# Performance work log

Hardware: AMD Instinct MI355X
Metric: run time of the kernel (lower is better)

The kernel has to match this reference:

```python
import jax, jax.numpy as jnp
import numpy as np

T = 32768          # number of t_eval points, dt = 30 s
BATCH = 32         # batched initial conditions
N_ROOMS = 16
N_STATE = N_ROOMS + 2
HID = 16
T0 = 259200.0      # start time (seconds); kept small so fp32 resolves 30 s steps
DT_GRID = 30.0
MU, STD = 23.359, 1.41      # state normalization for policy input
Q_VALUE = -16914.0          # cooling power per unit action
DAY = 86400.0
WEEK = 604800.0
A_SCALE, A_DIAG, B_SCALE = 1e-4, 1e-3, 1e-6


def setup_inputs() -> dict:
    key = jax.random.key(0)
    ks = jax.random.split(key, 8)
    t_eval = (T0 + DT_GRID * jnp.arange(T)).astype(jnp.float32)
    iv = 26.0 + jax.random.normal(ks[0], (BATCH, N_STATE), jnp.float32)
    W_A = jax.random.normal(ks[1], (N_STATE, N_STATE), jnp.float32)
    W_B = jax.random.normal(ks[2], (N_STATE, 1 + N_ROOMS), jnp.float32)
    W1 = jax.random.normal(ks[3], (HID, N_STATE + 2), jnp.float32)
    b1 = jax.random.normal(ks[4], (HID,), jnp.float32)
    w2 = jax.random.normal(ks[5], (HID,), jnp.float32)
    b2 = jax.random.normal(ks[6], (1,), jnp.float32)
    # outside-temperature table on a 30 s grid covering t_eval plus the +600 s tail
    Tout_table = 10.0 + 10.0 * jax.random.uniform(ks[7], (T + 21,), jnp.float32)
    return dict(t_eval=t_eval, iv=iv, W_A=W_A, W_B=W_B, W1=W1, b1=b1,
                w2=w2, b2=b2, Tout_table=Tout_table)


def reference(t_eval, iv, W_A, W_B, W1, b1, w2, b2, Tout_table):
    n = iv.shape[-1]
    A = A_SCALE * W_A - A_DIAG * jnp.eye(n, dtype=W_A.dtype)   # stable dynamics
    Bm = B_SCALE * W_B                                         # [n, 1+n_rooms]
    b_tout = Bm[:, 0]                                          # Tout column of B
    b_rooms = Q_VALUE * jnp.sum(Bm[:, 1:], axis=1)             # B @ (Q*ones) per unit action
    t0 = t_eval[0]
    nT = Tout_table.shape[0]

    def tout(t):  # linear interp of outside temperature at absolute time t
        pos = (t - t0) / DT_GRID
        i = jnp.clip(jnp.floor(pos).astype(jnp.int32), 0, nT - 2)
        fr = pos - i.astype(pos.dtype)
        return (1.0 - fr) * Tout_table[i] + fr * Tout_table[i + 1]

    def policy(t, x):  # deterministic cooling action in (0,1), per batch element
        tod = jnp.mod(t, DAY) / DAY
        tow = jnp.mod(t + 3.0 * DAY, WEEK) / WEEK   # epoch day 0 is a Thursday
        feats = jnp.broadcast_to(jnp.stack([tow, tod]).astype(x.dtype), (x.shape[0], 2))
        s = jnp.concatenate([(x - MU) / STD, feats], axis=1)   # [B, n+2]
        h = jnp.tanh(s @ W1.T + b1)
        return jax.nn.sigmoid(h @ w2 + b2[0])                  # [B]

    def f(t, x, act):  # dx/dt = A x + B u,  u = [Tout, Q*ones(n_rooms)]
        Bu = tout(t) * b_tout[None, :] + act[:, None] * b_rooms[None, :]
        return x @ A.T + Bu

    def step(x, ts):  # one fixed-step RK4 step; action held over the step (>=30 s gate)
        t, tn = ts
        dt = tn - t
        act = policy(t, x)
        k1 = f(t, x, act)
        k2 = f(t + 0.5 * dt, x + 0.5 * dt * k1, act)
        k3 = f(t + 0.5 * dt, x + 0.5 * dt * k2, act)
        k4 = f(tn, x + dt * k3, act)
        xn = x + (dt / 6.0) * (k1 + 2.0 * k2 + 2.0 * k3 + k4)
        return xn, xn

    _, xs = jax.lax.scan(step, iv, (t_eval[:-1], t_eval[1:]))
    return jnp.concatenate([iv[None], xs], axis=0)   # [T, batch, n_state]
```

## Files before the change

kernel.cpp:

```cpp
#include <hip/hip_runtime.h>

#define NSTATE 18
#define NBATCH 32
#define TSTEPS 32768
#define SEGS   64
#define SEGLEN 512
#define BURN   192

typedef float v2f __attribute__((ext_vector_type(2)));

#define PKFMA_LO(ACC, Gp, Xp) \
  asm("v_pk_fma_f32 %0, %1, %2, %0 op_sel:[0,0,0] op_sel_hi:[1,0,1]" \
      : "+v"(ACC) : "v"(Gp), "v"(Xp))
#define PKFMA_HI(ACC, Gp, Xp) \
  asm("v_pk_fma_f32 %0, %1, %2, %0 op_sel:[0,1,0] op_sel_hi:[1,1,1]" \
      : "+v"(ACC) : "v"(Gp), "v"(Xp))

template <int CTRL>
__device__ __forceinline__ float dpp_xadd(float x) {
  int y = __builtin_amdgcn_update_dpp(0, __float_as_int(x), CTRL, 0xF, 0xF, true);
  return x + __int_as_float(y);
}

#define STEPP(XI, XO, TIN, TNX, P, DOSTORE)                                       \
  do {                                                                            \
    TNX = *(const v2f*)(ldsT + 2 * (P) + 2);          \
    float fw = (float)uw, ft = (float)ut;                                         \
    float ilo = fmaf(TIN.x, C0.x, fmaf(TIN.y, C1.x, CBlo));                       \
    ilo = fmaf(fw, CWlo, ilo);                                                    \
    ilo = fmaf(ft, CTlo, ilo);                                                    \
    ilo = fmaf(a0p, F0.x, ilo);                                                   \
    ilo = fmaf(a1p, F1.x, ilo);                                                   \
    float ihi = fmaf(TIN.x, C0.y, TIN.y * C1.y);                                  \
    ihi = fmaf(a0p, F0.y, ihi);                                                   \
    ihi = fmaf(a1p, F1.y, ihi);                                                   \
    ilo = fmaf(TNX.x, C2lo, ilo);         \
    v2f accA; accA.x = ilo; accA.y = ihi;                                         \
    v2f accB; accB.x = 0.0f; accB.y = 0.0f;                                       \
    PKFMA_LO(accA, G[0],  XI[0]);  PKFMA_HI(accB, G[1],  XI[0]);                  \
    PKFMA_LO(accA, G[2],  XI[1]);  PKFMA_HI(accB, G[3],  XI[1]);                  \
    PKFMA_LO(accA, G[4],  XI[2]);  PKFMA_HI(accB, G[5],  XI[2]);                  \
    PKFMA_LO(accA, G[6],  XI[3]);  PKFMA_HI(accB, G[7],  XI[3]);                  \
    PKFMA_LO(accA, G[8],  XI[4]);  PKFMA_HI(accB, G[9],  XI[4]);                  \
    PKFMA_LO(accA, G[10], XI[5]);  PKFMA_HI(accB, G[11], XI[5]);                  \
    PKFMA_LO(accA, G[12], XI[6]);  PKFMA_HI(accB, G[13], XI[6]);                  \
    PKFMA_LO(accA, G[14], XI[7]);  PKFMA_HI(accB, G[15], XI[7]);                  \
    PKFMA_LO(accA, G[16], XI[8]);  PKFMA_HI(accB, G[17], XI[8]);                  \
    v2f acc = accA + accB;                                                        \
    float vlo = acc.x, vhi = acc.y;                                               \
    xbuf[wIdx] = vlo;              \
    XO[0] = *(const v2f*)(xbuf + 0);  XO[1] = *(const v2f*)(xbuf + 2);            \
    XO[2] = *(const v2f*)(xbuf + 4);  XO[3] = *(const v2f*)(xbuf + 6);            \
    XO[4] = *(const v2f*)(xbuf + 8);  XO[5] = *(const v2f*)(xbuf + 10);           \
    XO[6] = *(const v2f*)(xbuf + 12); XO[7] = *(const v2f*)(xbuf + 14);           \
    XO[8] = *(const v2f*)(xbuf + 16);                                             \
    float e2 = exp2f(vlo);                                                        \
    float rc = __builtin_amdgcn_rcpf(1.0f + e2);                                  \
    float pA = fmaf(nw2A, rc, w2A);                                               \
    pA = dpp_xadd<0xB1>(pA); pA = dpp_xadd<0x4E>(pA);                             \
    pA = dpp_xadd<0x141>(pA); pA = dpp_xadd<0x140>(pA);                           \
    float ez = exp2f(fmaf(pA, -1.44269504f, nb2));                                \
    float an = __builtin_amdgcn_rcpf(1.0f + ez);                                  \
    float aj0 = __int_as_float(__builtin_amdgcn_readlane(__float_as_int(an), 32));\
    float qB = fmaf(aj0, uB, vlo);                                                \
    float e2b = exp2f(qB);                                                        \
    float rcb = __builtin_amdgcn_rcpf(1.0f + e2b);                                \
    float pB = fmaf(nw2B, rcb, w2B);                                              \
    pB = dpp_xadd<0xB1>(pB); pB = dpp_xadd<0x4E>(pB);                             \
    pB = dpp_xadd<0x141>(pB); pB = dpp_xadd<0x140>(pB);                           \
    float ezb = exp2f(fmaf(pB, -1.44269504f, nb2));                               \
    float anb = __builtin_amdgcn_rcpf(1.0f + ezb);                                \
    float aj1 = __int_as_float(__builtin_amdgcn_readlane(__float_as_int(anb), 48));\
    if (DOSTORE) {                                                                \
      if (L < NSTATE) {                                                           \
        ob[L] = fmaf(aj0, cact, vhi);                               \
        ob[L + 576] = fmaf(aj1, cact, fmaf(aj0, pcact, vlo));       \
      }                                                                            \
      ob += 1152;                                                                 \
    }                                                                             \
    a0p = aj0; a1p = aj1;                                                         \
    ut += 60u; if (ut >= 86400u) ut -= 86400u;                                    \
    uw += 60u; if (uw >= 604800u) uw -= 604800u;                                  \
  } while (0)

__global__ __launch_bounds__(64) void rc_run(
    const float* __restrict__ WA, const float* __restrict__ WB,
    const float* __restrict__ W1, const float* __restrict__ b1,
    const float* __restrict__ w2, const float* __restrict__ b2,
    const float* __restrict__ iv, const float* __restrict__ tout,
    float* __restrict__ out) {
  __shared__ double DB[1440];
  double* A   = DB;
  double* A2  = DB + 324;
  double* A3  = DB + 648;
  double* A4  = DB + 972;
  double* bt  = DB + 1296;
  double* br  = DB + 1314;
  double* cv  = DB + 1332;
  double* d0v = DB + 1350;
  double* d1v = DB + 1368;
  double* pc1 = DB + 1386;
  double* pc2 = DB + 1404;
  double* pc3 = DB + 1422;
  __shared__ __align__(16) float xbuf[96];

  const int L = threadIdx.x;
  const int idx = blockIdx.x;
  const int b = idx & (NBATCH - 1);
  const int s = idx >> 5;
  const double dt = 30.0;
  const float PS = 2.88539008f;

  const int ks = (s == SEGS - 1) ? (TSTEPS - 1 - SEGLEN) : s * SEGLEN;
  const int kb = max(0, ks - BURN);
  const int mBurn = ks - kb;
  const int mEnd = (ks + SEGLEN) - kb;

  for (int t = L; t < 324; t += 64) {
    int i = t / 18, j = t % 18;
    A[t] = 1e-4 * (double)WA[t] - (i == j ? 1e-3 : 0.0);
  }
  if (L < NSTATE) {
    bt[L] = 1e-6 * (double)WB[L * 17 + 0];
    double ssum = 0.0;
    for (int c = 1; c < 17; ++c) ssum += (double)WB[L * 17 + c];
    br[L] = -16914.0 * 1e-6 * ssum;
  }
  __syncthreads();
  for (int t = L; t < 324; t += 64) {
    int i = t / 18, j = t % 18;
    double s2 = 0.0;
    for (int l = 0; l < 18; ++l) s2 += A[i * 18 + l] * A[l * 18 + j];
    A2[t] = s2;
  }
  __syncthreads();
  for (int t = L; t < 324; t += 64) {
    int i = t / 18, j = t % 18;
    double s3 = 0.0, s4 = 0.0;
    for (int l = 0; l < 18; ++l) {
      s3 += A2[i * 18 + l] * A[l * 18 + j];
      s4 += A2[i * 18 + l] * A2[l * 18 + j];
    }
    A3[t] = s3;
    A4[t] = s4;
  }
  __syncthreads();
  if (L < NSTATE) {
    double sc = 0.0, dd0 = 0.0, dd1 = 0.0;
    for (int j = 0; j < 18; ++j) {
      double m = (dt / 6.0) * ((L == j ? 6.0 : 0.0) + 3.0 * dt * A[L * 18 + j] +
                               dt * dt * A2[L * 18 + j] +
                               0.25 * dt * dt * dt * A3[L * 18 + j]);
      sc += m * br[j];
      double m1 = (dt / 6.0) * ((L == j ? 1.0 : 0.0) + dt * A[L * 18 + j] +
                                0.5 * dt * dt * A2[L * 18 + j] +
                                0.25 * dt * dt * dt * A3[L * 18 + j]);
      double m23 = (dt / 6.0) * ((L == j ? 4.0 : 0.0) + 2.0 * dt * A[L * 18 + j] +
                                 0.5 * dt * dt * A2[L * 18 + j]);
      double m4 = (L == j ? dt / 6.0 : 0.0);
      dd0 += (m1 + 0.5 * m23) * bt[j];
      dd1 += (0.5 * m23 + m4) * bt[j];
    }
    cv[L] = sc;
    d0v[L] = dd0;
    d1v[L] = dd1;
  }
  __syncthreads();
  for (int t = L; t < 324; t += 64) {
    int i = t / 18, j = t % 18;
    A[t] = (i == j ? 1.0 : 0.0) + dt * A[t] + (dt * dt / 2.0) * A2[t] +
           (dt * dt * dt / 6.0) * A3[t] + (dt * dt * dt * dt / 24.0) * A4[t];
  }
  __syncthreads();
  for (int t = L; t < 324; t += 64) {
    int i = t / 18, j = t % 18;
    double s2 = 0.0;
    for (int l = 0; l < 18; ++l) s2 += A[i * 18 + l] * A[l * 18 + j];
    A2[t] = s2;
  }
  __syncthreads();
  if (L < NSTATE) { double s1 = 0.0; for (int j = 0; j < 18; ++j) s1 += A[L * 18 + j] * cv[j];  pc1[L] = s1; }
  __syncthreads();
  if (L < NSTATE) { double s1 = 0.0; for (int j = 0; j < 18; ++j) s1 += A[L * 18 + j] * pc1[j]; pc2[L] = s1; }
  __syncthreads();
  if (L < NSTATE) { double s1 = 0.0; for (int j = 0; j < 18; ++j) s1 += A[L * 18 + j] * pc2[j]; pc3[L] = s1; }
  __syncthreads();

  v2f G[18];
  v2f F0; F0.x = 0.f; F0.y = 0.f;
  v2f F1; F1.x = 0.f; F1.y = 0.f;
  v2f C0; C0.x = 0.f; C0.y = 0.f;
  v2f C1; C1.x = 0.f; C1.y = 0.f;
  float C2lo = 0.f, CWlo = 0.f, CTlo = 0.f, CBlo = 0.f;
  float cact = 0.f, pcact = 0.f, uB = 0.f;
  float w2A = 0.f, nw2A = 0.f, w2B = 0.f, nw2B = 0.f;
  const float b2v = b2[0];
  const float nb2 = -1.44269504f * b2v;

  if (L < NSTATE) {
    for (int j = 0; j < 18; ++j) { G[j].x = (float)A2[L * 18 + j]; G[j].y = (float)A[L * 18 + j]; }
    double pd0 = 0.0, pd1 = 0.0;
    for (int j = 0; j < 18; ++j) { pd0 += A[L * 18 + j] * d0v[j]; pd1 += A[L * 18 + j] * d1v[j]; }
    C0.x = (float)pd0;            C0.y = (float)d0v[L];
    C1.x = (float)(pd1 + d0v[L]); C1.y = (float)d1v[L];
    C2lo = (float)d1v[L];
    F0.x = (float)pc3[L]; F0.y = (float)pc2[L];
    F1.x = (float)pc2[L]; F1.y = (float)pc1[L];
    cact = (float)cv[L];
    pcact = (float)pc1[L];
  } else if (L >= 32 && L < 48) {
    int m = L - 32;
    double f0 = 0.0, f1 = 0.0, ssum = 0.0;
    for (int j = 0; j < 18; ++j) {
      double g = (double)W1[m * 20 + j] * ((double)PS / 1.41);
      G[j].x = (float)g; G[j].y = 0.f;
      f0 += g * pc1[j];
      f1 += g * cv[j];
      ssum += (double)W1[m * 20 + j];
    }
    F0.x = (float)f0; F1.x = (float)f1;
    CBlo = (float)(((double)b1[m] - ssum * (23.359 / 1.41)) * (double)PS);
    CWlo = W1[m * 20 + 18] * PS * (1.0f / 604800.0f);
    CTlo = W1[m * 20 + 19] * PS * (1.0f / 86400.0f);
    w2A = w2[m]; nw2A = -2.0f * w2A;
  } else if (L >= 48) {
    int m = L - 48;
    double f0 = 0.0, f1 = 0.0, ub = 0.0, ssum = 0.0, wd0 = 0.0, wd1 = 0.0;
    for (int j = 0; j < 18; ++j) {
      double g = (double)W1[m * 20 + j] * ((double)PS / 1.41);
      double wp = 0.0;
      for (int k = 0; k < 18; ++k)
        wp += (double)W1[m * 20 + k] * ((double)PS / 1.41) * A[k * 18 + j];
      G[j].x = (float)wp; G[j].y = 0.f;
      f0 += g * pc2[j];
      f1 += g * pc1[j];
      ub += g * cv[j];
      wd0 += g * d0v[j];
      wd1 += g * d1v[j];
      ssum += (double)W1[m * 20 + j];
    }
    F0.x = (float)f0; F1.x = (float)f1; uB = (float)ub;
    C0.x = (float)wd0; C1.x = (float)wd1;
    CWlo = W1[m * 20 + 18] * PS * (1.0f / 604800.0f);
    CTlo = W1[m * 20 + 19] * PS * (1.0f / 86400.0f);
    CBlo = (float)(((double)b1[m] - ssum * (23.359 / 1.41)) * (double)PS) +
           30.0f * CWlo + 30.0f * CTlo;
    w2B = w2[m]; nw2B = -2.0f * w2B;
  } else {
    for (int j = 0; j < 18; ++j) { G[j].x = 0.f; G[j].y = 0.f; }
  }
  __syncthreads();

  float* ldsT = (float*)DB;
  const int cnt = mEnd + 2;
  for (int i = L; i < cnt; i += 64) ldsT[i] = tout[kb + i];
  __syncthreads();

  float q = (L < NSTATE) ? iv[b * NSTATE + L] : 0.0f;
  if (s == 0 && L < NSTATE) out[b * NSTATE + L] = q;

  float a0p = 0.0f, a1p = 0.0f;
  unsigned ut = (30u * (unsigned)kb) % 86400u;
  unsigned uw = (518400u + 30u * (unsigned)kb) % 604800u;

  float* ob = out + (size_t)(ks + 1) * (NBATCH * NSTATE) + b * NSTATE;

  const int wIdx = (L < NSTATE) ? L : (32 + L);
  xbuf[wIdx] = q;
  v2f X[9], Y[9];
  X[0] = *(const v2f*)(xbuf + 0);  X[1] = *(const v2f*)(xbuf + 2);
  X[2] = *(const v2f*)(xbuf + 4);  X[3] = *(const v2f*)(xbuf + 6);
  X[4] = *(const v2f*)(xbuf + 8);  X[5] = *(const v2f*)(xbuf + 10);
  X[6] = *(const v2f*)(xbuf + 12); X[7] = *(const v2f*)(xbuf + 14);
  X[8] = *(const v2f*)(xbuf + 16);

  v2f tU, tV;
  tU.x = ldsT[0]; tU.y = ldsT[1];

  const int nburn = mBurn >> 1;
  const int ntot = mEnd >> 1;
  int p = 0;
  for (; p < nburn; p += 2) {
    STEPP(X, Y, tU, tV, p, false);
    STEPP(Y, X, tV, tU, p + 1, false);
  }
  for (; p < ntot; p += 2) {
    STEPP(X, Y, tU, tV, p, true);
    STEPP(Y, X, tV, tU, p + 1, true);
  }
}

extern "C" void kernel_launch(void* const* d_in, const int* in_sizes, int n_in,
                              void* d_out, int out_size, void* d_ws, size_t ws_size,
                              hipStream_t stream) {
  const float* iv = (const float*)d_in[1];
  const float* WA = (const float*)d_in[2];
  const float* WB = (const float*)d_in[3];
  const float* W1 = (const float*)d_in[4];
  const float* b1 = (const float*)d_in[5];
  const float* w2 = (const float*)d_in[6];
  const float* b2 = (const float*)d_in[7];
  const float* tout = (const float*)d_in[8];
  float* out = (float*)d_out;

  rc_run<<<NBATCH * SEGS, 64, 0, stream>>>(WA, WB, W1, b1, w2, b2, iv, tout, out);
}
```

Measured before the change: 261.6 us.

## Delay action feedback by one extra double-step to shorten the serial critical path

Reworks the recurrence so the state update uses actions from two double-steps back, folded in through precomputed powers of the propagator (pc4, pc5). The most recent actions enter only as a scalar correction to the policy pre-activation and to the stored outputs. This takes the previous step's sigmoid/DPP-reduction chain off the dependency path of the matrix-vector FMA chain, so consecutive steps can overlap. In exchange it adds a few FMAs per step, more setup matrix-vector products, and extra registers.

```diff
diff --git a/kernel.cpp b/kernel.cpp
--- a/kernel.cpp
+++ b/kernel.cpp
@@ -22,19 +22,33 @@
   return x + __int_as_float(y);
 }
 
-#define STEPP(XI, XO, TIN, TNX, P, DOSTORE)                                       \
+#define TAIL(Q, AOUT, W2V, NW2V, LANE)                                            \
+  {                                                                               \
+    float e_ = exp2f(Q);                                                          \
+    float rc_ = __builtin_amdgcn_rcpf(1.0f + e_);                                 \
+    float p_ = fmaf(NW2V, rc_, W2V);                                              \
+    p_ = dpp_xadd<0xB1>(p_);                                                      \
+    p_ = dpp_xadd<0x4E>(p_);                                                      \
+    p_ = dpp_xadd<0x141>(p_);                                                     \
+    p_ = dpp_xadd<0x140>(p_);                                                     \
+    float ez_ = exp2f(fmaf(p_, -1.44269504f, nb2));                               \
+    float an_ = __builtin_amdgcn_rcpf(1.0f + ez_);                                \
+    AOUT = __int_as_float(__builtin_amdgcn_readlane(__float_as_int(an_), LANE));  \
+  }
+
+#define STEPP(XI, XO, TIN, TNX, P, DOSTORE, PP0, PP1, PR0, PR1)                   \
   do {                                                                            \
     TNX = *(const v2f*)(ldsT + 2 * (P) + 2);          \
     float fw = (float)uw, ft = (float)ut;                                         \
     float ilo = fmaf(TIN.x, C0.x, fmaf(TIN.y, C1.x, CBlo));                       \
     ilo = fmaf(fw, CWlo, ilo);                                                    \
     ilo = fmaf(ft, CTlo, ilo);                                                    \
-    ilo = fmaf(a0p, F0.x, ilo);                                                   \
-    ilo = fmaf(a1p, F1.x, ilo);                                                   \
+    ilo = fmaf(PP0, F0.x, ilo);        \
+    ilo = fmaf(PP1, F1.x, ilo);                                                   \
     float ihi = fmaf(TIN.x, C0.y, TIN.y * C1.y);                                  \
-    ihi = fmaf(a0p, F0.y, ihi);                                                   \
-    ihi = fmaf(a1p, F1.y, ihi);                                                   \
-    ilo = fmaf(TNX.x, C2lo, ilo);         \
+    ihi = fmaf(PP0, F0.y, ihi);                                                   \
+    ihi = fmaf(PP1, F1.y, ihi);                                                   \
+    ilo = fmaf(TNX.x, C2lo, ilo);                                                 \
     v2f accA; accA.x = ilo; accA.y = ihi;                                         \
     v2f accB; accB.x = 0.0f; accB.y = 0.0f;                                       \
     PKFMA_LO(accA, G[0],  XI[0]);  PKFMA_HI(accB, G[1],  XI[0]);                  \
@@ -54,31 +68,21 @@
     XO[4] = *(const v2f*)(xbuf + 8);  XO[5] = *(const v2f*)(xbuf + 10);           \
     XO[6] = *(const v2f*)(xbuf + 12); XO[7] = *(const v2f*)(xbuf + 14);           \
     XO[8] = *(const v2f*)(xbuf + 16);                                             \
-    float e2 = exp2f(vlo);                                                        \
-    float rc = __builtin_amdgcn_rcpf(1.0f + e2);                                  \
-    float pA = fmaf(nw2A, rc, w2A);                                               \
-    pA = dpp_xadd<0xB1>(pA); pA = dpp_xadd<0x4E>(pA);                             \
-    pA = dpp_xadd<0x141>(pA); pA = dpp_xadd<0x140>(pA);                           \
-    float ez = exp2f(fmaf(pA, -1.44269504f, nb2));                                \
-    float an = __builtin_amdgcn_rcpf(1.0f + ez);                                  \
-    float aj0 = __int_as_float(__builtin_amdgcn_readlane(__float_as_int(an), 32));\
-    float qB = fmaf(aj0, uB, vlo);                                                \
-    float e2b = exp2f(qB);                                                        \
-    float rcb = __builtin_amdgcn_rcpf(1.0f + e2b);                                \
-    float pB = fmaf(nw2B, rcb, w2B);                                              \
-    pB = dpp_xadd<0xB1>(pB); pB = dpp_xadd<0x4E>(pB);                             \
-    pB = dpp_xadd<0x141>(pB); pB = dpp_xadd<0x140>(pB);                           \
-    float ezb = exp2f(fmaf(pB, -1.44269504f, nb2));                               \
-    float anb = __builtin_amdgcn_rcpf(1.0f + ezb);                                \
-    float aj1 = __int_as_float(__builtin_amdgcn_readlane(__float_as_int(anb), 48));\
+                     \
+    float q0 = fmaf(PR0, PAv.x, fmaf(PR1, PAv.y, vlo));                           \
+    float aj0, aj1;                                                               \
+    TAIL(q0, aj0, w2A, nw2A, 32);                                                 \
+    float qB = fmaf(aj0, uB, q0);                                                 \
+    TAIL(qB, aj1, w2B, nw2B, 48);                                                 \
     if (DOSTORE) {                                                                \
       if (L < NSTATE) {                                                           \
-        ob[L] = fmaf(aj0, cact, vhi);                               \
-        ob[L + 576] = fmaf(aj1, cact, fmaf(aj0, pcact, vlo));       \
-      }                                                                            \
+        ob[L] = fmaf(aj0, cact, fmaf(PR0, Q0.x, fmaf(PR1, Q1.x, vhi)));           \
+        ob[L + 576] = fmaf(aj1, cact,                                             \
+                           fmaf(aj0, pcact, fmaf(PR0, Q0.y, fmaf(PR1, Q1.y, vlo)))); \
+      }                                                                           \
       ob += 1152;                                                                 \
     }                                                                             \
-    a0p = aj0; a1p = aj1;                                                         \
+    PP0 = aj0; PP1 = aj1;         \
     ut += 60u; if (ut >= 86400u) ut -= 86400u;                                    \
     uw += 60u; if (uw >= 604800u) uw -= 604800u;                                  \
   } while (0)
@@ -89,7 +93,7 @@
     const float* __restrict__ w2, const float* __restrict__ b2,
     const float* __restrict__ iv, const float* __restrict__ tout,
     float* __restrict__ out) {
-  __shared__ double DB[1440];
+  __shared__ double DB[1476];
   double* A   = DB;
   double* A2  = DB + 324;
   double* A3  = DB + 648;
@@ -102,6 +106,8 @@
   double* pc1 = DB + 1386;
   double* pc2 = DB + 1404;
   double* pc3 = DB + 1422;
+  double* pc4 = DB + 1440;
+  double* pc5 = DB + 1458;
   __shared__ __align__(16) float xbuf[96];
 
   const int L = threadIdx.x;
@@ -185,10 +191,17 @@
   __syncthreads();
   if (L < NSTATE) { double s1 = 0.0; for (int j = 0; j < 18; ++j) s1 += A[L * 18 + j] * pc2[j]; pc3[L] = s1; }
   __syncthreads();
+  if (L < NSTATE) { double s1 = 0.0; for (int j = 0; j < 18; ++j) s1 += A[L * 18 + j] * pc3[j]; pc4[L] = s1; }
+  __syncthreads();
+  if (L < NSTATE) { double s1 = 0.0; for (int j = 0; j < 18; ++j) s1 += A[L * 18 + j] * pc4[j]; pc5[L] = s1; }
+  __syncthreads();
 
   v2f G[18];
   v2f F0; F0.x = 0.f; F0.y = 0.f;
   v2f F1; F1.x = 0.f; F1.y = 0.f;
+  v2f PAv; PAv.x = 0.f; PAv.y = 0.f;
+  v2f Q0; Q0.x = 0.f; Q0.y = 0.f;
+  v2f Q1; Q1.x = 0.f; Q1.y = 0.f;
   v2f C0; C0.x = 0.f; C0.y = 0.f;
   v2f C1; C1.x = 0.f; C1.y = 0.f;
   float C2lo = 0.f, CWlo = 0.f, CTlo = 0.f, CBlo = 0.f;
@@ -204,42 +217,52 @@
     C0.x = (float)pd0;            C0.y = (float)d0v[L];
     C1.x = (float)(pd1 + d0v[L]); C1.y = (float)d1v[L];
     C2lo = (float)d1v[L];
-    F0.x = (float)pc3[L]; F0.y = (float)pc2[L];
-    F1.x = (float)pc2[L]; F1.y = (float)pc1[L];
+    F0.x = (float)pc5[L]; F0.y = (float)pc4[L];
+    F1.x = (float)pc4[L]; F1.y = (float)pc3[L];
+    Q0.x = (float)pc2[L]; Q0.y = (float)pc3[L];
+    Q1.x = (float)pc1[L]; Q1.y = (float)pc2[L];
     cact = (float)cv[L];
     pcact = (float)pc1[L];
   } else if (L >= 32 && L < 48) {
     int m = L - 32;
-    double f0 = 0.0, f1 = 0.0, ssum = 0.0;
+    double f0 = 0.0, f1 = 0.0, pa0 = 0.0, pa1 = 0.0, ssum = 0.0;
     for (int j = 0; j < 18; ++j) {
       double g = (double)W1[m * 20 + j] * ((double)PS / 1.41);
       G[j].x = (float)g; G[j].y = 0.f;
-      f0 += g * pc1[j];
-      f1 += g * cv[j];
+      f0 += g * pc3[j];
+      f1 += g * pc2[j];
+      pa0 += g * pc1[j];
+      pa1 += g * cv[j];
       ssum += (double)W1[m * 20 + j];
     }
     F0.x = (float)f0; F1.x = (float)f1;
+    PAv.x = (float)pa0; PAv.y = (float)pa1;
     CBlo = (float)(((double)b1[m] - ssum * (23.359 / 1.41)) * (double)PS);
     CWlo = W1[m * 20 + 18] * PS * (1.0f / 604800.0f);
     CTlo = W1[m * 20 + 19] * PS * (1.0f / 86400.0f);
     w2A = w2[m]; nw2A = -2.0f * w2A;
   } else if (L >= 48) {
     int m = L - 48;
-    double f0 = 0.0, f1 = 0.0, ub = 0.0, ssum = 0.0, wd0 = 0.0, wd1 = 0.0;
+    double f0 = 0.0, f1 = 0.0, pa0 = 0.0, pa1 = 0.0, ub = 0.0, ssum = 0.0,
+           wd0 = 0.0, wd1 = 0.0;
     for (int j = 0; j < 18; ++j) {
       double g = (double)W1[m * 20 + j] * ((double)PS / 1.41);
       double wp = 0.0;
       for (int k = 0; k < 18; ++k)
         wp += (double)W1[m * 20 + k] * ((double)PS / 1.41) * A[k * 18 + j];
       G[j].x = (float)wp; G[j].y = 0.f;
-      f0 += g * pc2[j];
-      f1 += g * pc1[j];
+      f0 += g * pc4[j];
+      f1 += g * pc3[j];
+      pa0 += g * pc2[j];
+      pa1 += g * pc1[j];
       ub += g * cv[j];
       wd0 += g * d0v[j];
       wd1 += g * d1v[j];
       ssum += (double)W1[m * 20 + j];
     }
-    F0.x = (float)f0; F1.x = (float)f1; uB = (float)ub;
+    F0.x = (float)f0; F1.x = (float)f1;
+    PAv.x = (float)pa0; PAv.y = (float)pa1;
+    uB = (float)ub;
     C0.x = (float)wd0; C1.x = (float)wd1;
     CWlo = W1[m * 20 + 18] * PS * (1.0f / 604800.0f);
     CTlo = W1[m * 20 + 19] * PS * (1.0f / 86400.0f);
@@ -259,7 +282,7 @@
   float q = (L < NSTATE) ? iv[b * NSTATE + L] : 0.0f;
   if (s == 0 && L < NSTATE) out[b * NSTATE + L] = q;
 
-  float a0p = 0.0f, a1p = 0.0f;
+  float r0 = 0.0f, r1 = 0.0f, r2 = 0.0f, r3 = 0.0f;
   unsigned ut = (30u * (unsigned)kb) % 86400u;
   unsigned uw = (518400u + 30u * (unsigned)kb) % 604800u;
 
@@ -281,12 +304,12 @@
   const int ntot = mEnd >> 1;
   int p = 0;
   for (; p < nburn; p += 2) {
-    STEPP(X, Y, tU, tV, p, false);
-    STEPP(Y, X, tV, tU, p + 1, false);
+    STEPP(X, Y, tU, tV, p,     false, r0, r1, r2, r3);
+    STEPP(Y, X, tV, tU, p + 1, false, r2, r3, r0, r1);
   }
   for (; p < ntot; p += 2) {
-    STEPP(X, Y, tU, tV, p, true);
-    STEPP(Y, X, tV, tU, p + 1, true);
+    STEPP(X, Y, tU, tV, p,     true, r0, r1, r2, r3);
+    STEPP(Y, X, tV, tU, p + 1, true, r2, r3, r0, r1);
   }
 }
 
```

After: 263.7 us. Within noise of the previous version (+0.8%).
